# Kernel optimization log

Measured on AMD Instinct MI355X. Metric: run time of the kernel, lower is better.

The kernel has to match this reference:

```python
import jax, jax.numpy as jnp
import numpy as np

N = 100000      # nodes
E = 1600000     # edges (avg degree 16)
IN_DIM = 64
OUT_DIM = 128
BN_EPS = 1e-5


def setup_inputs() -> dict:
    key = jax.random.key(0)
    kx, ke, kw, kb, ks = jax.random.split(key, 5)
    x = jax.random.normal(kx, (N, IN_DIM), dtype=jnp.float32)
    edge_index = jax.random.randint(ke, (2, E), 0, N, dtype=jnp.int32)
    # GCNConv linear weight (no bias inside lin; conv bias separate)
    W = jax.random.normal(kw, (IN_DIM, OUT_DIM), dtype=jnp.float32) / np.sqrt(IN_DIM)
    bias = jax.random.normal(kb, (OUT_DIM,), dtype=jnp.float32) * 0.01
    # skip projection Linear(in_dim, out_dim, bias=False)
    skip_W = jax.random.normal(ks, (IN_DIM, OUT_DIM), dtype=jnp.float32) / np.sqrt(IN_DIM)
    # BatchNorm1d affine params (training-mode batch stats used in forward)
    gamma = jnp.ones((OUT_DIM,), dtype=jnp.float32)
    beta = jnp.zeros((OUT_DIM,), dtype=jnp.float32)
    return {"x": x, "edge_index": edge_index, "W": W, "bias": bias,
            "skip_W": skip_W, "gamma": gamma, "beta": beta}


def _gcn_forward(x, edge_index, W, bias, skip_W, gamma, beta):
    n = x.shape[0]
    # GCNConv, normalize=True, add_self_loops=True (PyG defaults)
    row, col = edge_index[0], edge_index[1]
    loop = jnp.arange(n, dtype=edge_index.dtype)
    row_f = jnp.concatenate([row, loop])   # source nodes
    col_f = jnp.concatenate([col, loop])   # target nodes

    xt = x @ W                             # [N, OUT]
    deg = jax.ops.segment_sum(jnp.ones_like(col_f, dtype=xt.dtype), col_f,
                              num_segments=n)          # >= 1 due to self loops
    dinv = jax.lax.rsqrt(deg)
    norm = dinv[row_f] * dinv[col_f]                    # [E+N]
    msgs = xt[row_f] * norm[:, None]                    # gather + scale
    out = jax.ops.segment_sum(msgs, col_f, num_segments=n) + bias

    # skip-sum (in_dim != out_dim -> project)
    out = out + x @ skip_W

    # BatchNorm1d (training-mode batch statistics), affine
    mean = out.mean(axis=0)
    var = out.var(axis=0)
    out = (out - mean) * jax.lax.rsqrt(var + BN_EPS) * gamma + beta

    # ReLU; dropout p=0.0 -> identity
    return jax.nn.relu(out)


def reference(x, edge_index, W, bias, skip_W, gamma, beta):
    return _gcn_forward(x, edge_index, W, bias, skip_W, gamma, beta)
```

## Files before the change

### kernel.cpp

```cpp
#include <hip/hip_runtime.h>


typedef unsigned short ushort;
typedef __bf16 bf16x8 __attribute__((ext_vector_type(8)));
typedef float f32x4 __attribute__((ext_vector_type(4)));
typedef float f32x2 __attribute__((ext_vector_type(2)));
typedef ushort u16x8 __attribute__((ext_vector_type(8)));

constexpr int N_NODES = 100000;
constexpr int N_PAD   = 100096;
constexpr int E_EDGES = 1600000;

constexpr int BUCK_SHIFT = 7;
constexpr int NBUCK   = (N_NODES + 127) / 128;
constexpr int CHUNK   = 4096;
constexpr int NCHUNK  = (E_EDGES + CHUNK - 1) / CHUNK;
constexpr int CAP     = 4096;
constexpr int SORT_CAP = 4096;
constexpr int GG      = 256;

constexpr size_t OFF_SCALE  = 0;
constexpr size_t OFF_DINV   = 256;
constexpr size_t OFF_ROWPTR = 100352;
constexpr size_t OFF_DEG    = 200448;
constexpr size_t OFF_GCNT   = 300544;
constexpr size_t OFF_BINNED = 301568;
constexpr size_t OFF_PART   = OFF_BINNED;
constexpr size_t OFF_A      = 3504640;
constexpr size_t OFF_PRE    = 9910784;
constexpr size_t OFF_XD8    = OFF_PRE;
constexpr size_t OFF_BT     = 16316928;

static __device__ __forceinline__ ushort f2bf(float f) {
    union { float f; unsigned u; } v; v.f = f;
    unsigned r = v.u + 0x7FFFu + ((v.u >> 16) & 1u);
    return (ushort)(r >> 16);
}
static __device__ __forceinline__ float bf2f(ushort u) {
    union { unsigned u; float f; } v; v.u = (unsigned)u << 16;
    return v.f;
}
static __device__ __forceinline__ unsigned pack_fp8x4(float a, float b, float c, float d) {
    int r = 0;
    r = __builtin_amdgcn_cvt_pk_fp8_f32(a, b, r, false);
    r = __builtin_amdgcn_cvt_pk_fp8_f32(c, d, r, true);
    return (unsigned)r;
}

__global__ __launch_bounds__(256) void k_init(const float* __restrict__ W,
                                              const float* __restrict__ skipW,
                                              ushort* __restrict__ Bt,
                                              int* __restrict__ gcnt) {
    int t = threadIdx.x;
    if (blockIdx.x == 0) {
        for (int b = t; b < NBUCK; b += 256) gcnt[b] = 0;
        return;
    }
    int idx = (blockIdx.x - 1) * 256 + t;
    int k = idx >> 7, n = idx & 127;
    float v = (k < 64) ? W[k * 128 + n] : skipW[(k - 64) * 128 + n];
    Bt[n * 128 + k] = f2bf(v);
}

__global__ __launch_bounds__(512) void k_scatter(const int* __restrict__ row,
                                                 const int* __restrict__ col,
                                                 int* __restrict__ gcnt,
                                                 unsigned int* __restrict__ binned) {
    __shared__ int h[NBUCK];
    __shared__ int bb[NBUCK];
    int c = blockIdx.x, t = threadIdx.x;
    for (int b = t; b < NBUCK; b += 512) h[b] = 0;
    __syncthreads();
    const int4* col4 = (const int4*)col;
    const int4* row4 = (const int4*)row;
    int g0 = c * (CHUNK / 4);
#pragma unroll
    for (int i = 0; i < CHUNK / 2048; ++i) {
        int g4 = g0 + i * 512 + t;
        if (g4 * 4 + 3 < E_EDGES) {
            int4 cc = col4[g4];
            atomicAdd(&h[cc.x >> BUCK_SHIFT], 1);
            atomicAdd(&h[cc.y >> BUCK_SHIFT], 1);
            atomicAdd(&h[cc.z >> BUCK_SHIFT], 1);
            atomicAdd(&h[cc.w >> BUCK_SHIFT], 1);
        } else {
#pragma unroll
            for (int j = 0; j < 4; ++j) {
                int e = g4 * 4 + j;
                if (e < E_EDGES) atomicAdd(&h[col[e] >> BUCK_SHIFT], 1);
            }
        }
    }
    __syncthreads();
    for (int b = t; b < NBUCK; b += 512) {
        int cb = h[b];
        bb[b] = cb ? atomicAdd(&gcnt[b], cb) : 0;
        h[b] = 0;
    }
    __syncthreads();
#pragma unroll
    for (int i = 0; i < CHUNK / 2048; ++i) {
        int g4 = g0 + i * 512 + t;
        if (g4 * 4 + 3 < E_EDGES) {
            int4 cc = col4[g4];
            int4 rr = row4[g4];
            int b, p;
            b = cc.x >> BUCK_SHIFT; p = bb[b] + atomicAdd(&h[b], 1);
            if (p < CAP) binned[(size_t)b * CAP + p] = ((unsigned)(cc.x & 127) << 17) | (unsigned)rr.x;
            b = cc.y >> BUCK_SHIFT; p = bb[b] + atomicAdd(&h[b], 1);
            if (p < CAP) binned[(size_t)b * CAP + p] = ((unsigned)(cc.y & 127) << 17) | (unsigned)rr.y;
            b = cc.z >> BUCK_SHIFT; p = bb[b] + atomicAdd(&h[b], 1);
            if (p < CAP) binned[(size_t)b * CAP + p] = ((unsigned)(cc.z & 127) << 17) | (unsigned)rr.z;
            b = cc.w >> BUCK_SHIFT; p = bb[b] + atomicAdd(&h[b], 1);
            if (p < CAP) binned[(size_t)b * CAP + p] = ((unsigned)(cc.w & 127) << 17) | (unsigned)rr.w;
        } else {
#pragma unroll
            for (int j = 0; j < 4; ++j) {
                int e = g4 * 4 + j;
                if (e < E_EDGES) {
                    int d = col[e], s = row[e];
                    int b = d >> BUCK_SHIFT;
                    int p = bb[b] + atomicAdd(&h[b], 1);
                    if (p < CAP) binned[(size_t)b * CAP + p] = ((unsigned)(d & 127) << 17) | (unsigned)s;
                }
            }
        }
    }
}

__global__ __launch_bounds__(256) void k_sortbucket(unsigned int* __restrict__ binned,
                                                    const int* __restrict__ gcnt,
                                                    int* __restrict__ rowptr,
                                                    int* __restrict__ deg,
                                                    float* __restrict__ dinv,
                                                    const float* __restrict__ x,
                                                    unsigned* __restrict__ xd8,
                                                    ushort* __restrict__ A) {
    __shared__ unsigned int ebuf[SORT_CAP];
    __shared__ int sbuf[SORT_CAP];
    __shared__ int lcnt[128];
    __shared__ int lptr[128];
    __shared__ float ldinv[128];
    __shared__ int wsum[2];
    int b = blockIdx.x, t = threadIdx.x;
    int i0 = b * CAP;
    int cnt = min(gcnt[b], CAP);
    int n0 = b << BUCK_SHIFT;
    int nn = min(128, N_NODES - n0);

    for (int k = t; k < cnt; k += 256) ebuf[k] = binned[i0 + k];
    if (t < 128) lcnt[t] = 0;
    __syncthreads();
    for (int k = t; k < cnt; k += 256) atomicAdd(&lcnt[ebuf[k] >> 17], 1);
    __syncthreads();

    int myc = 0, val = 0;
    if (t < 128) {
        myc = lcnt[t];
        val = myc;
#pragma unroll
        for (int d = 1; d < 64; d <<= 1) {
            int o = __shfl_up(val, d);
            if ((t & 63) >= d) val += o;
        }
        if ((t & 63) == 63) wsum[t >> 6] = val;
    }
    __syncthreads();
    if (t < 128) {
        if (t >= 64) val += wsum[0];
        int excl = val - myc;
        lptr[t] = excl;
        float dv = rsqrtf((float)myc + 1.0f);
        ldinv[t] = dv;
        if (t < nn) {
            rowptr[n0 + t] = i0 + excl;
            deg[n0 + t] = myc;
            dinv[n0 + t] = dv;
        }
    }
    __syncthreads();
    for (int k = t; k < cnt; k += 256) {
        unsigned int e = ebuf[k];
        int j = (int)(e >> 17);
        int p = atomicAdd(&lptr[j], 1);
        sbuf[p] = (int)(e & 0x1FFFF);
    }
    __syncthreads();
    for (int k = t; k < cnt; k += 256) binned[i0 + k] = (unsigned int)sbuf[k];

#pragma unroll
    for (int it = 0; it < 8; ++it) {
        int idx = it * 256 + t;
        int nl = idx >> 4, q = idx & 15;
        int c = n0 + nl;
        unsigned w8 = 0;
        ushort4 xb = {0, 0, 0, 0};
        if (nl < nn) {
            float4 v = ((const float4*)x)[(size_t)c * 16 + q];
            float d = ldinv[nl];
            w8 = pack_fp8x4(v.x * d, v.y * d, v.z * d, v.w * d);
            xb.x = f2bf(v.x); xb.y = f2bf(v.y); xb.z = f2bf(v.z); xb.w = f2bf(v.w);
        }
        xd8[(size_t)c * 16 + q] = w8;
        ((ushort4*)A)[(size_t)c * 32 + 16 + q] = xb;
    }
}

__global__ __launch_bounds__(256) void k_agg(const unsigned* __restrict__ xd8,
                                             const float* __restrict__ dinv,
                                             const int* __restrict__ rowptr,
                                             const int* __restrict__ deg,
                                             const unsigned int* __restrict__ csr,
                                             ushort* __restrict__ A) {
    int t = blockIdx.x * blockDim.x + threadIdx.x;
    if (t >= N_PAD * 16) return;
    int c = t >> 4;
    int q = t & 15;
    if (c >= N_NODES) {
        ushort4 z = {0, 0, 0, 0};
        ((ushort4*)A)[(size_t)c * 32 + q] = z;
        return;
    }
    float dc = dinv[c];
    float4 acc;
    {
        unsigned w = xd8[t];
        f32x2 lo = __builtin_amdgcn_cvt_pk_f32_fp8((int)w, false);
        f32x2 hi = __builtin_amdgcn_cvt_pk_f32_fp8((int)w, true);
        acc.x = lo.x; acc.y = lo.y; acc.z = hi.x; acc.w = hi.y;
    }
    int i0 = rowptr[c], i1 = i0 + deg[c];
    int i = i0;
    for (; i + 8 <= i1; i += 8) {
        int s[8];
#pragma unroll
        for (int k = 0; k < 8; ++k) s[k] = (int)csr[i + k];
        unsigned w[8];
#pragma unroll
        for (int k = 0; k < 8; ++k) w[k] = xd8[s[k] * 16 + q];
#pragma unroll
        for (int k = 0; k < 8; ++k) {
            f32x2 lo = __builtin_amdgcn_cvt_pk_f32_fp8((int)w[k], false);
            f32x2 hi = __builtin_amdgcn_cvt_pk_f32_fp8((int)w[k], true);
            acc.x += lo.x; acc.y += lo.y; acc.z += hi.x; acc.w += hi.y;
        }
    }
    for (; i < i1; ++i) {
        unsigned w = xd8[(int)csr[i] * 16 + q];
        f32x2 lo = __builtin_amdgcn_cvt_pk_f32_fp8((int)w, false);
        f32x2 hi = __builtin_amdgcn_cvt_pk_f32_fp8((int)w, true);
        acc.x += lo.x; acc.y += lo.y; acc.z += hi.x; acc.w += hi.y;
    }
    ushort4 o;
    o.x = f2bf(acc.x * dc); o.y = f2bf(acc.y * dc);
    o.z = f2bf(acc.z * dc); o.w = f2bf(acc.w * dc);
    ((ushort4*)A)[(size_t)c * 32 + q] = o;
}

__global__ __launch_bounds__(512, 2) void k_gemm(const ushort* __restrict__ A,
                                                 const ushort* __restrict__ Bt,
                                                 ushort* __restrict__ pre,
                                                 float* __restrict__ partial) {
    __shared__ float sred[128];
    __shared__ float qred[128];
    int tid = threadIdx.x;
    int wave = tid >> 6, lane = tid & 63;
    int wm = wave >> 2, wn = wave & 3;
    int l15 = lane & 15, quad = lane >> 4;
    int col0 = wn * 32;

    if (tid < 128) { sred[tid] = 0.f; qred[tid] = 0.f; }
    __syncthreads();

    bf16x8 bf_[4][2];
#pragma unroll
    for (int kc = 0; kc < 4; ++kc)
#pragma unroll
        for (int jc = 0; jc < 2; ++jc)
            bf_[kc][jc] = *(const bf16x8*)&Bt[(size_t)(col0 + jc * 16 + l15) * 128 + kc * 32 + quad * 8];

    float lsum[8] = {0.f, 0.f, 0.f, 0.f, 0.f, 0.f, 0.f, 0.f};
    float lsq[8]  = {0.f, 0.f, 0.f, 0.f, 0.f, 0.f, 0.f, 0.f};

    for (int ci = blockIdx.x; ci < NBUCK; ci += GG) {
        int row0 = ci * 128 + wm * 64;
        bf16x8 af[4][4];
#pragma unroll
        for (int kc = 0; kc < 4; ++kc)
#pragma unroll
            for (int ir = 0; ir < 4; ++ir)
                af[kc][ir] = *(const bf16x8*)&A[(size_t)(row0 + ir * 16 + l15) * 128 + kc * 32 + quad * 8];

        f32x4 acc[4][2];
#pragma unroll
        for (int ir = 0; ir < 4; ++ir)
#pragma unroll
            for (int jc = 0; jc < 2; ++jc) acc[ir][jc] = (f32x4){0.f, 0.f, 0.f, 0.f};

#pragma unroll
        for (int kc = 0; kc < 4; ++kc)
#pragma unroll
            for (int ir = 0; ir < 4; ++ir)
#pragma unroll
                for (int jc = 0; jc < 2; ++jc)
                    acc[ir][jc] = __builtin_amdgcn_mfma_f32_16x16x32_bf16(
                        bf_[kc][jc], af[kc][ir], acc[ir][jc], 0, 0, 0);

#pragma unroll
        for (int ir = 0; ir < 4; ++ir) {
            int row = row0 + ir * 16 + l15;
            bool live = row < N_NODES;
#pragma unroll
            for (int jc = 0; jc < 2; ++jc) {
                ushort4 o;
                o.x = f2bf(acc[ir][jc][0]); o.y = f2bf(acc[ir][jc][1]);
                o.z = f2bf(acc[ir][jc][2]); o.w = f2bf(acc[ir][jc][3]);
                *(ushort4*)&pre[(size_t)row * 128 + col0 + jc * 16 + quad * 4] = o;
                if (live) {
#pragma unroll
                    for (int r = 0; r < 4; ++r) {
                        float v = acc[ir][jc][r];
                        lsum[jc * 4 + r] += v;
                        lsq[jc * 4 + r]  += v * v;
                    }
                }
            }
        }
    }

#pragma unroll
    for (int m = 1; m < 16; m <<= 1) {
#pragma unroll
        for (int i = 0; i < 8; ++i) {
            lsum[i] += __shfl_xor(lsum[i], m);
            lsq[i]  += __shfl_xor(lsq[i], m);
        }
    }
    if (l15 == 0) {
#pragma unroll
        for (int jc = 0; jc < 2; ++jc)
#pragma unroll
            for (int r = 0; r < 4; ++r) {
                int c = col0 + jc * 16 + quad * 4 + r;
                atomicAdd(&sred[c], lsum[jc * 4 + r]);
                atomicAdd(&qred[c], lsq[jc * 4 + r]);
            }
    }
    __syncthreads();
    if (tid < 128) {
        partial[(size_t)blockIdx.x * 256 + tid]       = sred[tid];
        partial[(size_t)blockIdx.x * 256 + 128 + tid] = qred[tid];
    }
}

__global__ __launch_bounds__(256) void k_reduce(const float* __restrict__ partial,
                                                const float* __restrict__ gamma,
                                                const float* __restrict__ beta,
                                                float* __restrict__ scaleshift) {
    __shared__ float ls[256], lq[256];
    int j = blockIdx.x;
    int t = threadIdx.x;
    float s = 0.f, q = 0.f;
    for (int p = t; p < GG; p += 256) {
        s += partial[(size_t)p * 256 + j];
        q += partial[(size_t)p * 256 + 128 + j];
    }
    ls[t] = s; lq[t] = q;
    __syncthreads();
#pragma unroll
    for (int off = 128; off > 0; off >>= 1) {
        if (t < off) { ls[t] += ls[t + off]; lq[t] += lq[t + off]; }
        __syncthreads();
    }
    if (t == 0) {
        float mean = ls[0] * (1.0f / N_NODES);
        float var  = lq[0] * (1.0f / N_NODES) - mean * mean;
        float sc   = gamma[j] * rsqrtf(var + 1e-5f);
        scaleshift[j]       = sc;
        scaleshift[128 + j] = beta[j] - mean * sc;
    }
}

__global__ __launch_bounds__(256) void k_apply(const ushort* __restrict__ pre,
                                               float* __restrict__ out,
                                               const float* __restrict__ ss) {
    int t = blockIdx.x * blockDim.x + threadIdx.x;
    if (t >= N_NODES * 16) return;
    int j8 = t & 15;
    u16x8 p = ((const u16x8*)pre)[t];
    float4 sc0 = ((const float4*)ss)[j8 * 2];
    float4 sc1 = ((const float4*)ss)[j8 * 2 + 1];
    float4 sh0 = ((const float4*)(ss + 128))[j8 * 2];
    float4 sh1 = ((const float4*)(ss + 128))[j8 * 2 + 1];
    float4 v0, v1;
    v0.x = fmaxf(fmaf(bf2f(p[0]), sc0.x, sh0.x), 0.f);
    v0.y = fmaxf(fmaf(bf2f(p[1]), sc0.y, sh0.y), 0.f);
    v0.z = fmaxf(fmaf(bf2f(p[2]), sc0.z, sh0.z), 0.f);
    v0.w = fmaxf(fmaf(bf2f(p[3]), sc0.w, sh0.w), 0.f);
    v1.x = fmaxf(fmaf(bf2f(p[4]), sc1.x, sh1.x), 0.f);
    v1.y = fmaxf(fmaf(bf2f(p[5]), sc1.y, sh1.y), 0.f);
    v1.z = fmaxf(fmaf(bf2f(p[6]), sc1.z, sh1.z), 0.f);
    v1.w = fmaxf(fmaf(bf2f(p[7]), sc1.w, sh1.w), 0.f);
    ((float4*)out)[t * 2]     = v0;
    ((float4*)out)[t * 2 + 1] = v1;
}

extern "C" void kernel_launch(void* const* d_in, const int* in_sizes, int n_in,
                              void* d_out, int out_size, void* d_ws, size_t ws_size,
                              hipStream_t stream) {
    const float* x      = (const float*)d_in[0];
    const int*   eidx   = (const int*)d_in[1];
    const float* W      = (const float*)d_in[2];
    const float* skipW  = (const float*)d_in[4];
    const float* gamma  = (const float*)d_in[5];
    const float* beta   = (const float*)d_in[6];
    float* out = (float*)d_out;
    float* ws  = (float*)d_ws;

    const int* row = eidx;
    const int* col = eidx + E_EDGES;

    float* scaleshift = ws + OFF_SCALE;
    float* dinv       = ws + OFF_DINV;
    int*   rowptr     = (int*)(ws + OFF_ROWPTR);
    int*   deg        = (int*)(ws + OFF_DEG);
    int*   gcnt       = (int*)(ws + OFF_GCNT);
    unsigned int* binned = (unsigned int*)(ws + OFF_BINNED);
    float* partial    = ws + OFF_PART;
    ushort* A         = (ushort*)(ws + OFF_A);
    unsigned* xd8     = (unsigned*)(ws + OFF_XD8);
    ushort* pre       = (ushort*)(ws + OFF_PRE);
    ushort* Bt        = (ushort*)(ws + OFF_BT);

    k_init<<<65, 256, 0, stream>>>(W, skipW, Bt, gcnt);
    k_scatter<<<NCHUNK, 512, 0, stream>>>(row, col, gcnt, binned);
    k_sortbucket<<<NBUCK, 256, 0, stream>>>(binned, gcnt, rowptr, deg, dinv, x, xd8, A);
    k_agg<<<(N_PAD * 16 + 255) / 256, 256, 0, stream>>>(xd8, dinv, rowptr, deg, binned, A);
    k_gemm<<<GG, 512, 0, stream>>>(A, Bt, pre, partial);
    k_reduce<<<128, 256, 0, stream>>>(partial, gamma, beta, scaleshift);
    k_apply<<<(N_NODES * 16 + 255) / 256, 256, 0, stream>>>(pre, out, scaleshift);
}
```

Baseline: 195.0 us.

## Split fp8 feature table into two halves and aggregate each in a separate pass

The fp8 scaled-feature table is stored as two separate 32-byte-per-node arrays, one for each half of the 64 input features. Aggregation runs as two launches, each gathering only one half. The intent is to shrink the working set of each gather pass (about 3.2 MB per half) so it stays resident in cache and random neighbor gathers hit more often. In exchange, the CSR indices, rowptr and deg are read twice, there is an extra launch, and each gathered row is only 32 bytes.

```diff
diff --git a/kernel.cpp b/kernel.cpp
--- a/kernel.cpp
+++ b/kernel.cpp
@@ -28,7 +28,8 @@
 constexpr size_t OFF_PART   = OFF_BINNED;
 constexpr size_t OFF_A      = 3504640;
 constexpr size_t OFF_PRE    = 9910784;
-constexpr size_t OFF_XD8    = OFF_PRE;
+constexpr size_t OFF_XD8A   = OFF_PRE;
+constexpr size_t OFF_XD8B   = OFF_PRE + 800768;
 constexpr size_t OFF_BT     = 16316928;
 
 static __device__ __forceinline__ ushort f2bf(float f) {
@@ -134,7 +135,8 @@
                                                     int* __restrict__ deg,
                                                     float* __restrict__ dinv,
                                                     const float* __restrict__ x,
-                                                    unsigned* __restrict__ xd8,
+                                                    unsigned* __restrict__ xd8a,
+                                                    unsigned* __restrict__ xd8b,
                                                     ushort* __restrict__ A) {
     __shared__ unsigned int ebuf[SORT_CAP];
     __shared__ int sbuf[SORT_CAP];
@@ -201,30 +203,32 @@
             w8 = pack_fp8x4(v.x * d, v.y * d, v.z * d, v.w * d);
             xb.x = f2bf(v.x); xb.y = f2bf(v.y); xb.z = f2bf(v.z); xb.w = f2bf(v.w);
         }
-        xd8[(size_t)c * 16 + q] = w8;
+        if (q < 8) xd8a[(size_t)c * 8 + q] = w8;
+        else       xd8b[(size_t)c * 8 + (q - 8)] = w8;
         ((ushort4*)A)[(size_t)c * 32 + 16 + q] = xb;
     }
 }
 
-__global__ __launch_bounds__(256) void k_agg(const unsigned* __restrict__ xd8,
-                                             const float* __restrict__ dinv,
-                                             const int* __restrict__ rowptr,
-                                             const int* __restrict__ deg,
-                                             const unsigned int* __restrict__ csr,
-                                             ushort* __restrict__ A) {
+__global__ __launch_bounds__(256) void k_agg_half(const unsigned* __restrict__ tab,
+                                                  const float* __restrict__ dinv,
+                                                  const int* __restrict__ rowptr,
+                                                  const int* __restrict__ deg,
+                                                  const unsigned int* __restrict__ csr,
+                                                  ushort* __restrict__ A,
+                                                  int woff) {
     int t = blockIdx.x * blockDim.x + threadIdx.x;
-    if (t >= N_PAD * 16) return;
-    int c = t >> 4;
-    int q = t & 15;
+    if (t >= N_PAD * 8) return;
+    int c = t >> 3;
+    int q = t & 7;
     if (c >= N_NODES) {
         ushort4 z = {0, 0, 0, 0};
-        ((ushort4*)A)[(size_t)c * 32 + q] = z;
+        ((ushort4*)A)[(size_t)c * 32 + woff + q] = z;
         return;
     }
     float dc = dinv[c];
     float4 acc;
     {
-        unsigned w = xd8[t];
+        unsigned w = tab[(size_t)c * 8 + q];
         f32x2 lo = __builtin_amdgcn_cvt_pk_f32_fp8((int)w, false);
         f32x2 hi = __builtin_amdgcn_cvt_pk_f32_fp8((int)w, true);
         acc.x = lo.x; acc.y = lo.y; acc.z = hi.x; acc.w = hi.y;
@@ -237,7 +241,7 @@
         for (int k = 0; k < 8; ++k) s[k] = (int)csr[i + k];
         unsigned w[8];
 #pragma unroll
-        for (int k = 0; k < 8; ++k) w[k] = xd8[s[k] * 16 + q];
+        for (int k = 0; k < 8; ++k) w[k] = tab[(size_t)s[k] * 8 + q];
 #pragma unroll
         for (int k = 0; k < 8; ++k) {
             f32x2 lo = __builtin_amdgcn_cvt_pk_f32_fp8((int)w[k], false);
@@ -246,7 +250,7 @@
         }
     }
     for (; i < i1; ++i) {
-        unsigned w = xd8[(int)csr[i] * 16 + q];
+        unsigned w = tab[(size_t)csr[i] * 8 + q];
         f32x2 lo = __builtin_amdgcn_cvt_pk_f32_fp8((int)w, false);
         f32x2 hi = __builtin_amdgcn_cvt_pk_f32_fp8((int)w, true);
         acc.x += lo.x; acc.y += lo.y; acc.z += hi.x; acc.w += hi.y;
@@ -254,7 +258,7 @@
     ushort4 o;
     o.x = f2bf(acc.x * dc); o.y = f2bf(acc.y * dc);
     o.z = f2bf(acc.z * dc); o.w = f2bf(acc.w * dc);
-    ((ushort4*)A)[(size_t)c * 32 + q] = o;
+    ((ushort4*)A)[(size_t)c * 32 + woff + q] = o;
 }
 
 __global__ __launch_bounds__(512, 2) void k_gemm(const ushort* __restrict__ A,
@@ -428,14 +432,16 @@
     unsigned int* binned = (unsigned int*)(ws + OFF_BINNED);
     float* partial    = ws + OFF_PART;
     ushort* A         = (ushort*)(ws + OFF_A);
-    unsigned* xd8     = (unsigned*)(ws + OFF_XD8);
+    unsigned* xd8a    = (unsigned*)(ws + OFF_XD8A);
+    unsigned* xd8b    = (unsigned*)(ws + OFF_XD8B);
     ushort* pre       = (ushort*)(ws + OFF_PRE);
     ushort* Bt        = (ushort*)(ws + OFF_BT);
 
     k_init<<<65, 256, 0, stream>>>(W, skipW, Bt, gcnt);
     k_scatter<<<NCHUNK, 512, 0, stream>>>(row, col, gcnt, binned);
-    k_sortbucket<<<NBUCK, 256, 0, stream>>>(binned, gcnt, rowptr, deg, dinv, x, xd8, A);
-    k_agg<<<(N_PAD * 16 + 255) / 256, 256, 0, stream>>>(xd8, dinv, rowptr, deg, binned, A);
+    k_sortbucket<<<NBUCK, 256, 0, stream>>>(binned, gcnt, rowptr, deg, dinv, x, xd8a, xd8b, A);
+    k_agg_half<<<(N_PAD * 8 + 255) / 256, 256, 0, stream>>>(xd8a, dinv, rowptr, deg, binned, A, 0);
+    k_agg_half<<<(N_PAD * 8 + 255) / 256, 256, 0, stream>>>(xd8b, dinv, rowptr, deg, binned, A, 8);
     k_gemm<<<GG, 512, 0, stream>>>(A, Bt, pre, partial);
     k_reduce<<<128, 256, 0, stream>>>(partial, gamma, beta, scaleshift);
     k_apply<<<(N_NODES * 16 + 255) / 256, 256, 0, stream>>>(pre, out, scaleshift);
```

After: 203.9 us. +4.6%, slower.
